# Kernel tuning notes

Hardware: AMD Instinct MI355X
Metric: run time of the kernel (lower is better)

The kernel has to match this reference:

```python
import jax, jax.numpy as jnp
import numpy as np

# Config: B=4, S=2048, E=512, H=8 heads, D=E//H=64, FF=2048.
# QLayer (quantum circuit) is replaced by its linear stand-in matching the
# declared I/O dims: V: D->D per head, Q/K: D->1 (scalar per token).

EPS = 1e-5

def layernorm(x):
    # torch LayerNorm(elementwise_affine=False), population variance
    mu = jnp.mean(x, axis=-1, keepdims=True)
    var = jnp.var(x, axis=-1, keepdims=True)
    return (x - mu) / jnp.sqrt(var + EPS)


def setup_inputs() -> dict:
    key = jax.random.key(0)
    ks = jax.random.split(key, 12)
    B, S, E, H = 4, 2048, 512, 8
    D = E // H
    F = 2048
    u = lambda k, shape, fan: jax.random.uniform(k, shape, jnp.float32, -1.0 / np.sqrt(fan), 1.0 / np.sqrt(fan))
    return {
        "input1": jax.random.normal(ks[0], (B, S, E), jnp.float32),
        # per-head value projection D->D
        "Wv": u(ks[1], (H, D, D), D),
        "bv": u(ks[2], (H, D), D),
        # per-head scalar query / key projections D->1
        "Wq": u(ks[3], (H, D), D),
        "bq": u(ks[4], (H,), D),
        "Wk": u(ks[5], (H, D), D),
        "bk": u(ks[6], (H,), D),
        # merger MLP: E->F (GELU) -> E
        "W1": u(ks[7], (E, F), E),
        "b1": u(ks[8], (F,), E),
        "W2": u(ks[9], (F, E), F),
        "b2": u(ks[10], (E,), F),
    }


def reference(input1, Wv, bv, Wq, bq, Wk, bk, W1, b1, W2, b2):
    B, S, E = input1.shape
    H, D, _ = Wv.shape
    x = layernorm(input1)
    # chunk along last dim == reshape into heads
    xh = x.reshape(B, S, H, D)
    # per-head projections (vectorized over heads)
    V = jnp.einsum('bshd,hde->bshe', xh, Wv) + bv            # [B,S,H,D]
    Q = jnp.einsum('bshd,hd->bhs', xh, Wq) + bq[None, :, None]  # [B,H,S]
    K = jnp.einsum('bshd,hd->bhs', xh, Wk) + bk[None, :, None]  # [B,H,S]
    # quadratic-distance scores: A = -(Q - K)^2, [B,H,S,S]
    A = -jnp.square(Q[:, :, :, None] - K[:, :, None, :])
    attn = jax.nn.softmax(A * (1.0 / np.sqrt(D)), axis=-1)
    head_out = jnp.einsum('bhqk,bkhd->bqhd', attn, V).reshape(B, S, E)
    # merger: Linear -> GELU (exact) -> Linear, plus residual
    h = jax.nn.gelu(head_out @ W1 + b1, approximate=False)
    return h @ W2 + b2 + input1
```

## Files before the change

### kernel.cpp

```cpp
#include <hip/hip_runtime.h>
#include <hip/hip_bf16.h>


#define Bsz 4
#define Ssz 2048
#define Esz 512
#define Hsz 8
#define Dsz 64
#define Fsz 2048
#define NR 16
#define NCH 16
#define CHK 128

typedef __attribute__((ext_vector_type(8))) short bf16x8;
typedef __attribute__((ext_vector_type(4))) float f32x4;

__device__ __constant__ float RS[16] = {
    0.f, 1.0f, 0.70710678f, 0.57735027f, 0.5f, 0.44721360f, 0.40824829f,
    0.37796447f, 0.35355339f, 0.33333333f, 0.31622777f, 0.30151134f,
    0.28867513f, 0.27735010f, 0.26726124f, 0.25819889f};

static __device__ __forceinline__ void gload_lds16(const void* g, void* l) {
    __builtin_amdgcn_global_load_lds(
        (const __attribute__((address_space(1))) unsigned int*)g,
        (__attribute__((address_space(3))) unsigned int*)l, 16, 0, 0);
}

static __device__ __forceinline__ unsigned short f2bf(float f) {
    unsigned int b = __float_as_uint(f);
    b += 0x7FFFu + ((b >> 16) & 1u);
    return (unsigned short)(b >> 16);
}

__global__ __launch_bounds__(256) void ln_qk_kernel(
    const float* __restrict__ x,
    const float* __restrict__ Wq, const float* __restrict__ bq,
    const float* __restrict__ Wk, const float* __restrict__ bk,
    float* __restrict__ Qo, float* __restrict__ Ko, __hip_bfloat16* __restrict__ Xn)
{
    int wid = threadIdx.x >> 6, lane = threadIdx.x & 63;
    int tok = blockIdx.x * 4 + wid;
    int b = tok >> 11, s = tok & 2047;

    const float* xrow = x + (size_t)tok * Esz;
    float4 v0 = *(const float4*)&xrow[lane * 8];
    float4 v1 = *(const float4*)&xrow[lane * 8 + 4];

    float sum = v0.x + v0.y + v0.z + v0.w + v1.x + v1.y + v1.z + v1.w;
    #pragma unroll
    for (int off = 32; off > 0; off >>= 1) sum += __shfl_xor(sum, off);
    float mean = sum * (1.0f / 512.0f);

    float d[8] = {v0.x - mean, v0.y - mean, v0.z - mean, v0.w - mean,
                  v1.x - mean, v1.y - mean, v1.z - mean, v1.w - mean};
    float ss = 0.f;
    #pragma unroll
    for (int j = 0; j < 8; ++j) ss = fmaf(d[j], d[j], ss);
    #pragma unroll
    for (int off = 32; off > 0; off >>= 1) ss += __shfl_xor(ss, off);
    float inv = rsqrtf(ss * (1.0f / 512.0f) + 1e-5f);

    float xn[8];
    #pragma unroll
    for (int j = 0; j < 8; ++j) xn[j] = d[j] * inv;

    int h = lane >> 3, dsub = (lane & 7) * 8;
    union { bf16x8 v; unsigned short u[8]; } pk;
    #pragma unroll
    for (int j = 0; j < 8; ++j) pk.u[j] = f2bf(xn[j]);
    *(bf16x8*)((unsigned short*)Xn + (((size_t)(b * Hsz + h) * Ssz + s) * Dsz + dsub)) = pk.v;

    float4 wqa = *(const float4*)&Wq[h * 64 + dsub];
    float4 wqb = *(const float4*)&Wq[h * 64 + dsub + 4];
    float4 wka = *(const float4*)&Wk[h * 64 + dsub];
    float4 wkb = *(const float4*)&Wk[h * 64 + dsub + 4];
    float pq = xn[0]*wqa.x + xn[1]*wqa.y + xn[2]*wqa.z + xn[3]*wqa.w
             + xn[4]*wqb.x + xn[5]*wqb.y + xn[6]*wqb.z + xn[7]*wqb.w;
    float pkv = xn[0]*wka.x + xn[1]*wka.y + xn[2]*wka.z + xn[3]*wka.w
              + xn[4]*wkb.x + xn[5]*wkb.y + xn[6]*wkb.z + xn[7]*wkb.w;
    #pragma unroll
    for (int off = 1; off < 8; off <<= 1) {
        pq  += __shfl_xor(pq, off);
        pkv += __shfl_xor(pkv, off);
    }
    if ((lane & 7) == 0) {
        int bh = b * Hsz + h;
        Qo[bh * Ssz + s] = pq + bq[h];
        Ko[bh * Ssz + s] = pkv + bk[h];
    }
}

__global__ __launch_bounds__(256) void attn_moments(
    const float* __restrict__ Kv, const __hip_bfloat16* __restrict__ Xn, float* __restrict__ Gp)
{
    int chunk = blockIdx.x, bh = blockIdx.y;
    int t = threadIdx.x;
    __shared__ float Wt[CHK][17];
    __shared__ float denp[4][16];

    if (t < CHK) {
        float kv = Kv[bh * Ssz + chunk * CHK + t];
        float wn = __expf(-0.125f * kv * kv);
        float half = 0.5f * kv;
        Wt[t][0] = wn;
        #pragma unroll
        for (int n = 1; n < NR; ++n) { wn *= half * RS[n]; Wt[t][n] = wn; }
    }
    __syncthreads();

    int w = t >> 6, lane = t & 63;
    int ng = w * 4;
    float a0 = 0.f, a1 = 0.f, a2 = 0.f, a3 = 0.f;
    const __hip_bfloat16* xb = Xn + ((size_t)bh * Ssz + chunk * CHK) * Dsz + lane;
    for (int k = 0; k < CHK; ++k) {
        float v = __bfloat162float(xb[(size_t)k * Dsz]);
        a0 = fmaf(Wt[k][ng + 0], v, a0);
        a1 = fmaf(Wt[k][ng + 1], v, a1);
        a2 = fmaf(Wt[k][ng + 2], v, a2);
        a3 = fmaf(Wt[k][ng + 3], v, a3);
    }
    size_t base = (((size_t)bh * NCH + chunk) * NR + ng) * 68 + lane;
    Gp[base + 0 * 68] = a0;
    Gp[base + 1 * 68] = a1;
    Gp[base + 2 * 68] = a2;
    Gp[base + 3 * 68] = a3;

    if (t < 64) {
        int n = t & 15, q = t >> 4;
        float s = 0.f;
        #pragma unroll
        for (int kk = 0; kk < CHK / 4; ++kk) s += Wt[q * (CHK / 4) + kk][n];
        denp[q][n] = s;
    }
    __syncthreads();
    if (t < 16) {
        float m = denp[0][t] + denp[1][t] + denp[2][t] + denp[3][t];
        Gp[(((size_t)bh * NCH + chunk) * NR + t) * 68 + 64] = m;
    }
}

__global__ __launch_bounds__(256) void attn_mtransform(
    const float* __restrict__ Gp, const float* __restrict__ Wv, const float* __restrict__ bv,
    float* __restrict__ M)
{
    int bh = blockIdx.x, h = bh & 7, t = threadIdx.x;
    __shared__ float Gf[NR * 68];
    for (int i = t; i < NR * 68; i += 256) {
        float s = 0.f;
        #pragma unroll
        for (int c = 0; c < NCH; ++c)
            s += Gp[(((size_t)bh * NCH + c) * NR) * 68 + i];
        Gf[i] = s;
    }
    __syncthreads();
    #pragma unroll
    for (int rep = 0; rep < 4; ++rep) {
        int o = t + rep * 256;
        int n = o >> 6, dd = o & 63;
        float den = Gf[n * 68 + 64];
        float acc = den * bv[h * 64 + dd];
        const float* wv = Wv + ((size_t)h * 64) * 64 + dd;
        #pragma unroll
        for (int e = 0; e < 64; ++e) acc = fmaf(Gf[n * 68 + e], wv[(size_t)e * 64], acc);
        M[(size_t)bh * NR * 68 + n * 68 + dd] = acc;
        if (dd == 0) M[(size_t)bh * NR * 68 + n * 68 + 64] = den;
    }
}

__global__ __launch_bounds__(256) void attn_apply(
    const float* __restrict__ Qv, const float* __restrict__ M, __hip_bfloat16* __restrict__ A1)
{
    int tok = blockIdx.x;
    int b = tok >> 11, s = tok & 2047;
    int t = threadIdx.x;
    #pragma unroll
    for (int rep = 0; rep < 2; ++rep) {
        int e = t + rep * 256;
        int h = e >> 6, dd = e & 63;
        int bh = b * 8 + h;
        float q = Qv[bh * Ssz + s];
        const float* Mb = M + (size_t)bh * NR * 68;
        float half = 0.5f * q;
        float phi = 1.0f;
        float num = Mb[dd], den = Mb[64];
        #pragma unroll
        for (int n = 1; n < NR; ++n) {
            phi *= half * RS[n];
            num = fmaf(phi, Mb[n * 68 + dd], num);
            den = fmaf(phi, Mb[n * 68 + 64], den);
        }
        A1[(size_t)tok * Esz + e] = __float2bfloat16(num / den);
    }
}

__global__ __launch_bounds__(256) void transpose_bf16(
    const float* __restrict__ in, __hip_bfloat16* __restrict__ out, int R, int C)
{
    __shared__ float tile[32][33];
    int bx = blockIdx.x, by = blockIdx.y;
    int t = threadIdx.x;
    int tc = t & 31, tr = t >> 5;
    #pragma unroll
    for (int i = 0; i < 4; ++i) {
        int r = by * 32 + tr + i * 8, c = bx * 32 + tc;
        tile[tr + i * 8][tc] = in[(size_t)r * C + c];
    }
    __syncthreads();
    #pragma unroll
    for (int i = 0; i < 4; ++i) {
        int ro = bx * 32 + tr + i * 8, co = by * 32 + tc;
        out[(size_t)ro * R + co] = __float2bfloat16(tile[tc][tr + i * 8]);
    }
}

template <int KDIM, int EPI>
__global__ __launch_bounds__(256) void gemm_bf16(
    const __hip_bfloat16* __restrict__ A, const __hip_bfloat16* __restrict__ Bt,
    const float* __restrict__ bias, const float* __restrict__ resid,
    void* __restrict__ Out, int N)
{
    __shared__ unsigned short As[128][32];
    __shared__ unsigned short Bs[128][32];
    int t = threadIdx.x;
    int w = t >> 6, lane = t & 63;
    int wr = w >> 1, wc = w & 1;
    int bm = blockIdx.y * 128, bn = blockIdx.x * 128;

    f32x4 acc[4][4] = {};
    const int r = t >> 2, cg = (t & 3) * 8;

    for (int k0 = 0; k0 < KDIM; k0 += 32) {
        gload_lds16(&A[(size_t)(bm + r) * KDIM + k0 + cg], &As[r][cg]);
        gload_lds16(&A[(size_t)(bm + r + 64) * KDIM + k0 + cg], &As[r + 64][cg]);
        gload_lds16(&Bt[(size_t)(bn + r) * KDIM + k0 + cg], &Bs[r][cg]);
        gload_lds16(&Bt[(size_t)(bn + r + 64) * KDIM + k0 + cg], &Bs[r + 64][cg]);
        __syncthreads();
        bf16x8 af[4], bfr[4];
        #pragma unroll
        for (int i = 0; i < 4; ++i) {
            af[i]  = *(const bf16x8*)&As[wr * 64 + i * 16 + (lane & 15)][(lane >> 4) * 8];
            bfr[i] = *(const bf16x8*)&Bs[wc * 64 + i * 16 + (lane & 15)][(lane >> 4) * 8];
        }
        #pragma unroll
        for (int i = 0; i < 4; ++i)
            #pragma unroll
            for (int j = 0; j < 4; ++j)
                acc[i][j] = __builtin_amdgcn_mfma_f32_16x16x32_bf16(af[i], bfr[j], acc[i][j], 0, 0, 0);
        __syncthreads();
    }

    int col0 = lane & 15, rowg = lane >> 4;
    #pragma unroll
    for (int i = 0; i < 4; ++i) {
        #pragma unroll
        for (int j = 0; j < 4; ++j) {
            #pragma unroll
            for (int v = 0; v < 4; ++v) {
                int m = bm + wr * 64 + i * 16 + rowg * 4 + v;
                int n = bn + wc * 64 + j * 16 + col0;
                float val = acc[i][j][v] + bias[n];
                if (EPI == 0) {
                    float g = 0.5f * val * (1.0f + erff(val * 0.70710678f));
                    ((__hip_bfloat16*)Out)[(size_t)m * N + n] = __float2bfloat16(g);
                } else {
                    size_t idx = (size_t)m * N + n;
                    ((float*)Out)[idx] = val + resid[idx];
                }
            }
        }
    }
}

extern "C" void kernel_launch(void* const* d_in, const int* in_sizes, int n_in,
                              void* d_out, int out_size, void* d_ws, size_t ws_size,
                              hipStream_t stream) {
    const float* x  = (const float*)d_in[0];
    const float* Wv = (const float*)d_in[1];
    const float* bv = (const float*)d_in[2];
    const float* Wq = (const float*)d_in[3];
    const float* bq = (const float*)d_in[4];
    const float* Wk = (const float*)d_in[5];
    const float* bk = (const float*)d_in[6];
    const float* W1 = (const float*)d_in[7];
    const float* b1 = (const float*)d_in[8];
    const float* W2 = (const float*)d_in[9];
    const float* b2 = (const float*)d_in[10];
    float* out = (float*)d_out;

    char* ws = (char*)d_ws;
    float* Qb    = (float*)(ws + 0);
    float* Kb    = (float*)(ws + 262144);
    __hip_bfloat16* Xn = (__hip_bfloat16*)(ws + 524288);
    float* Gp    = (float*)(ws + 8912896);
    float* Mfull = (float*)(ws + 11141120);
    __hip_bfloat16* A1   = (__hip_bfloat16*)(ws + 11280384);
    __hip_bfloat16* W1T  = (__hip_bfloat16*)(ws + 19668992);
    __hip_bfloat16* W2T  = (__hip_bfloat16*)(ws + 21766144);
    __hip_bfloat16* hbuf = (__hip_bfloat16*)(ws + 23863296);

    ln_qk_kernel<<<dim3((Bsz * Ssz) / 4), 256, 0, stream>>>(x, Wq, bq, Wk, bk, Qb, Kb, Xn);
    attn_moments<<<dim3(NCH, Bsz * Hsz), 256, 0, stream>>>(Kb, Xn, Gp);
    attn_mtransform<<<dim3(Bsz * Hsz), 256, 0, stream>>>(Gp, Wv, bv, Mfull);
    attn_apply<<<dim3(Bsz * Ssz), 256, 0, stream>>>(Qb, Mfull, A1);
    transpose_bf16<<<dim3(Fsz / 32, Esz / 32), 256, 0, stream>>>(W1, W1T, Esz, Fsz);
    transpose_bf16<<<dim3(Esz / 32, Fsz / 32), 256, 0, stream>>>(W2, W2T, Fsz, Esz);
    gemm_bf16<Esz, 0><<<dim3(Fsz / 128, (Bsz * Ssz) / 128), 256, 0, stream>>>(A1, W1T, b1, nullptr, hbuf, Fsz);
    gemm_bf16<Fsz, 1><<<dim3(Esz / 128, (Bsz * Ssz) / 128), 256, 0, stream>>>(hbuf, W2T, b2, x, out, Esz);
}
```

Before: 210.1 us.

## Fuse prep kernels, merge moments with transform, pipeline GEMMs with triple buffering

Folds layernorm/QK projection and both weight transposes into one prep kernel. Merges the moment computation with the Wv transform using a last-block atomic counter, and vectorizes the moment inner loop with bf16x8 loads and shuffle reductions. Rewrites the GEMM with a 3-stage LDS pipeline using explicit vmcnt waits, a swizzled block order for L2 locality, and a 64-wide N tile for the second GEMM to raise block count. This cuts launches and hides global-load latency, at the cost of more LDS per block and a hand-tuned wait sequence that depends on the exact number of loads in flight.

```diff
diff --git a/kernel.cpp b/kernel.cpp
--- a/kernel.cpp
+++ b/kernel.cpp
@@ -31,75 +31,115 @@
     b += 0x7FFFu + ((b >> 16) & 1u);
     return (unsigned short)(b >> 16);
 }
-
-__global__ __launch_bounds__(256) void ln_qk_kernel(
+static __device__ __forceinline__ float bf2f(unsigned short u) {
+    return __int_as_float(((int)u) << 16);
+}
+
+__global__ __launch_bounds__(256) void prep_kernel(
     const float* __restrict__ x,
     const float* __restrict__ Wq, const float* __restrict__ bq,
     const float* __restrict__ Wk, const float* __restrict__ bk,
-    float* __restrict__ Qo, float* __restrict__ Ko, __hip_bfloat16* __restrict__ Xn)
+    const float* __restrict__ W1, const float* __restrict__ W2,
+    float* __restrict__ Qo, float* __restrict__ Ko, __hip_bfloat16* __restrict__ Xn,
+    __hip_bfloat16* __restrict__ W1T, __hip_bfloat16* __restrict__ W2T)
 {
-    int wid = threadIdx.x >> 6, lane = threadIdx.x & 63;
-    int tok = blockIdx.x * 4 + wid;
-    int b = tok >> 11, s = tok & 2047;
-
-    const float* xrow = x + (size_t)tok * Esz;
-    float4 v0 = *(const float4*)&xrow[lane * 8];
-    float4 v1 = *(const float4*)&xrow[lane * 8 + 4];
-
-    float sum = v0.x + v0.y + v0.z + v0.w + v1.x + v1.y + v1.z + v1.w;
-    #pragma unroll
-    for (int off = 32; off > 0; off >>= 1) sum += __shfl_xor(sum, off);
-    float mean = sum * (1.0f / 512.0f);
-
-    float d[8] = {v0.x - mean, v0.y - mean, v0.z - mean, v0.w - mean,
-                  v1.x - mean, v1.y - mean, v1.z - mean, v1.w - mean};
-    float ss = 0.f;
-    #pragma unroll
-    for (int j = 0; j < 8; ++j) ss = fmaf(d[j], d[j], ss);
-    #pragma unroll
-    for (int off = 32; off > 0; off >>= 1) ss += __shfl_xor(ss, off);
-    float inv = rsqrtf(ss * (1.0f / 512.0f) + 1e-5f);
-
-    float xn[8];
-    #pragma unroll
-    for (int j = 0; j < 8; ++j) xn[j] = d[j] * inv;
-
-    int h = lane >> 3, dsub = (lane & 7) * 8;
-    union { bf16x8 v; unsigned short u[8]; } pk;
-    #pragma unroll
-    for (int j = 0; j < 8; ++j) pk.u[j] = f2bf(xn[j]);
-    *(bf16x8*)((unsigned short*)Xn + (((size_t)(b * Hsz + h) * Ssz + s) * Dsz + dsub)) = pk.v;
-
-    float4 wqa = *(const float4*)&Wq[h * 64 + dsub];
-    float4 wqb = *(const float4*)&Wq[h * 64 + dsub + 4];
-    float4 wka = *(const float4*)&Wk[h * 64 + dsub];
-    float4 wkb = *(const float4*)&Wk[h * 64 + dsub + 4];
-    float pq = xn[0]*wqa.x + xn[1]*wqa.y + xn[2]*wqa.z + xn[3]*wqa.w
-             + xn[4]*wqb.x + xn[5]*wqb.y + xn[6]*wqb.z + xn[7]*wqb.w;
-    float pkv = xn[0]*wka.x + xn[1]*wka.y + xn[2]*wka.z + xn[3]*wka.w
-              + xn[4]*wkb.x + xn[5]*wkb.y + xn[6]*wkb.z + xn[7]*wkb.w;
-    #pragma unroll
-    for (int off = 1; off < 8; off <<= 1) {
-        pq  += __shfl_xor(pq, off);
-        pkv += __shfl_xor(pkv, off);
-    }
-    if ((lane & 7) == 0) {
-        int bh = b * Hsz + h;
-        Qo[bh * Ssz + s] = pq + bq[h];
-        Ko[bh * Ssz + s] = pkv + bk[h];
-    }
-}
-
-__global__ __launch_bounds__(256) void attn_moments(
-    const float* __restrict__ Kv, const __hip_bfloat16* __restrict__ Xn, float* __restrict__ Gp)
+    int bid = blockIdx.x;
+    if (bid < 2048) {
+        int wid = threadIdx.x >> 6, lane = threadIdx.x & 63;
+        int tok = bid * 4 + wid;
+        int b = tok >> 11, s = tok & 2047;
+
+        const float* xrow = x + (size_t)tok * Esz;
+        float4 v0 = *(const float4*)&xrow[lane * 8];
+        float4 v1 = *(const float4*)&xrow[lane * 8 + 4];
+
+        float sum = v0.x + v0.y + v0.z + v0.w + v1.x + v1.y + v1.z + v1.w;
+        #pragma unroll
+        for (int off = 32; off > 0; off >>= 1) sum += __shfl_xor(sum, off);
+        float mean = sum * (1.0f / 512.0f);
+
+        float d[8] = {v0.x - mean, v0.y - mean, v0.z - mean, v0.w - mean,
+                      v1.x - mean, v1.y - mean, v1.z - mean, v1.w - mean};
+        float ss = 0.f;
+        #pragma unroll
+        for (int j = 0; j < 8; ++j) ss = fmaf(d[j], d[j], ss);
+        #pragma unroll
+        for (int off = 32; off > 0; off >>= 1) ss += __shfl_xor(ss, off);
+        float inv = rsqrtf(ss * (1.0f / 512.0f) + 1e-5f);
+
+        float xn[8];
+        #pragma unroll
+        for (int j = 0; j < 8; ++j) xn[j] = d[j] * inv;
+
+        int h = lane >> 3, dsub = (lane & 7) * 8;
+        union { bf16x8 v; unsigned short u[8]; } pk;
+        #pragma unroll
+        for (int j = 0; j < 8; ++j) pk.u[j] = f2bf(xn[j]);
+        *(bf16x8*)((unsigned short*)Xn + (((size_t)(b * Hsz + h) * Ssz + s) * Dsz + dsub)) = pk.v;
+
+        float4 wqa = *(const float4*)&Wq[h * 64 + dsub];
+        float4 wqb = *(const float4*)&Wq[h * 64 + dsub + 4];
+        float4 wka = *(const float4*)&Wk[h * 64 + dsub];
+        float4 wkb = *(const float4*)&Wk[h * 64 + dsub + 4];
+        float pq = xn[0]*wqa.x + xn[1]*wqa.y + xn[2]*wqa.z + xn[3]*wqa.w
+                 + xn[4]*wqb.x + xn[5]*wqb.y + xn[6]*wqb.z + xn[7]*wqb.w;
+        float pkv = xn[0]*wka.x + xn[1]*wka.y + xn[2]*wka.z + xn[3]*wka.w
+                  + xn[4]*wkb.x + xn[5]*wkb.y + xn[6]*wkb.z + xn[7]*wkb.w;
+        #pragma unroll
+        for (int off = 1; off < 8; off <<= 1) {
+            pq  += __shfl_xor(pq, off);
+            pkv += __shfl_xor(pkv, off);
+        }
+        if ((lane & 7) == 0) {
+            int bh = b * Hsz + h;
+            Qo[bh * Ssz + s] = pq + bq[h];
+            Ko[bh * Ssz + s] = pkv + bk[h];
+        }
+        return;
+    }
+
+    __shared__ float tile[32][33];
+    const float* in;
+    __hip_bfloat16* outp;
+    int R, C, bx, by;
+    if (bid < 3072) {
+        int tb = bid - 2048;
+        in = W1; outp = W1T; R = Esz; C = Fsz;
+        bx = tb & 63; by = tb >> 6;
+    } else {
+        int tb = bid - 3072;
+        in = W2; outp = W2T; R = Fsz; C = Esz;
+        bx = tb & 15; by = tb >> 4;
+    }
+    int t = threadIdx.x;
+    int tc = t & 31, tr = t >> 5;
+    #pragma unroll
+    for (int i = 0; i < 4; ++i) {
+        int rr = by * 32 + tr + i * 8, cc = bx * 32 + tc;
+        tile[tr + i * 8][tc] = in[(size_t)rr * C + cc];
+    }
+    __syncthreads();
+    #pragma unroll
+    for (int i = 0; i < 4; ++i) {
+        int ro = bx * 32 + tr + i * 8, co = by * 32 + tc;
+        outp[(size_t)ro * R + co] = __float2bfloat16(tile[tc][tr + i * 8]);
+    }
+}
+
+__global__ __launch_bounds__(256) void attn_moments_fused(
+    const float* __restrict__ Kv, const __hip_bfloat16* __restrict__ Xn,
+    const float* __restrict__ Wv, const float* __restrict__ bvp,
+    float* __restrict__ Gp, float* __restrict__ M, unsigned int* __restrict__ cnt)
 {
-    int chunk = blockIdx.x, bh = blockIdx.y;
+    int bh = blockIdx.x >> 4, chunk = blockIdx.x & 15, h = bh & 7;
     int t = threadIdx.x;
     __shared__ float Wt[CHK][17];
-    __shared__ float denp[4][16];
-
+    __shared__ float Gf[NR * 68];
+    __shared__ int isLast;
+
+    int k0 = chunk * CHK;
     if (t < CHK) {
-        float kv = Kv[bh * Ssz + chunk * CHK + t];
+        float kv = Kv[bh * Ssz + k0 + t];
         float wn = __expf(-0.125f * kv * kv);
         float half = 0.5f * kv;
         Wt[t][0] = wn;
@@ -109,42 +149,56 @@
     __syncthreads();
 
     int w = t >> 6, lane = t & 63;
+    int kk = lane >> 3, dg = lane & 7;
     int ng = w * 4;
-    float a0 = 0.f, a1 = 0.f, a2 = 0.f, a3 = 0.f;
-    const __hip_bfloat16* xb = Xn + ((size_t)bh * Ssz + chunk * CHK) * Dsz + lane;
-    for (int k = 0; k < CHK; ++k) {
-        float v = __bfloat162float(xb[(size_t)k * Dsz]);
-        a0 = fmaf(Wt[k][ng + 0], v, a0);
-        a1 = fmaf(Wt[k][ng + 1], v, a1);
-        a2 = fmaf(Wt[k][ng + 2], v, a2);
-        a3 = fmaf(Wt[k][ng + 3], v, a3);
-    }
-    size_t base = (((size_t)bh * NCH + chunk) * NR + ng) * 68 + lane;
-    Gp[base + 0 * 68] = a0;
-    Gp[base + 1 * 68] = a1;
-    Gp[base + 2 * 68] = a2;
-    Gp[base + 3 * 68] = a3;
-
-    if (t < 64) {
-        int n = t & 15, q = t >> 4;
+    float acc[4][8] = {};
+    const unsigned short* xb = (const unsigned short*)Xn + ((size_t)bh * Ssz + k0) * Dsz + dg * 8;
+    for (int kc = 0; kc < CHK / 8; ++kc) {
+        int kl = kc * 8 + kk;
+        bf16x8 xv = *(const bf16x8*)&xb[(size_t)kl * Dsz];
+        float xf[8];
+        #pragma unroll
+        for (int e = 0; e < 8; ++e) xf[e] = bf2f((unsigned short)xv[e]);
+        #pragma unroll
+        for (int n = 0; n < 4; ++n) {
+            float wt = Wt[kl][ng + n];
+            #pragma unroll
+            for (int e = 0; e < 8; ++e) acc[n][e] = fmaf(wt, xf[e], acc[n][e]);
+        }
+    }
+    #pragma unroll
+    for (int off = 8; off < 64; off <<= 1)
+        #pragma unroll
+        for (int n = 0; n < 4; ++n)
+            #pragma unroll
+            for (int e = 0; e < 8; ++e)
+                acc[n][e] += __shfl_xor(acc[n][e], off);
+    if (kk == 0) {
+        #pragma unroll
+        for (int n = 0; n < 4; ++n) {
+            float* gp = &Gp[(((size_t)bh * NCH + chunk) * NR + ng + n) * 68 + dg * 8];
+            float4 lo = {acc[n][0], acc[n][1], acc[n][2], acc[n][3]};
+            float4 hi = {acc[n][4], acc[n][5], acc[n][6], acc[n][7]};
+            *(float4*)gp = lo;
+            *(float4*)(gp + 4) = hi;
+        }
+    }
+    if (t < NR) {
         float s = 0.f;
-        #pragma unroll
-        for (int kk = 0; kk < CHK / 4; ++kk) s += Wt[q * (CHK / 4) + kk][n];
-        denp[q][n] = s;
-    }
-    __syncthreads();
-    if (t < 16) {
-        float m = denp[0][t] + denp[1][t] + denp[2][t] + denp[3][t];
-        Gp[(((size_t)bh * NCH + chunk) * NR + t) * 68 + 64] = m;
-    }
-}
-
-__global__ __launch_bounds__(256) void attn_mtransform(
-    const float* __restrict__ Gp, const float* __restrict__ Wv, const float* __restrict__ bv,
-    float* __restrict__ M)
-{
-    int bh = blockIdx.x, h = bh & 7, t = threadIdx.x;
-    __shared__ float Gf[NR * 68];
+        for (int k = 0; k < CHK; ++k) s += Wt[k][t];
+        Gp[(((size_t)bh * NCH + chunk) * NR + t) * 68 + 64] = s;
+    }
+
+    __threadfence();
+    __syncthreads();
+    if (t == 0) {
+        unsigned int old = atomicAdd(&cnt[bh], 1u);
+        isLast = (old == NCH - 1) ? 1 : 0;
+    }
+    __syncthreads();
+    if (!isLast) return;
+    __threadfence();
+
     for (int i = t; i < NR * 68; i += 256) {
         float s = 0.f;
         #pragma unroll
@@ -158,11 +212,11 @@
         int o = t + rep * 256;
         int n = o >> 6, dd = o & 63;
         float den = Gf[n * 68 + 64];
-        float acc = den * bv[h * 64 + dd];
+        float accv = den * bvp[h * 64 + dd];
         const float* wv = Wv + ((size_t)h * 64) * 64 + dd;
         #pragma unroll
-        for (int e = 0; e < 64; ++e) acc = fmaf(Gf[n * 68 + e], wv[(size_t)e * 64], acc);
-        M[(size_t)bh * NR * 68 + n * 68 + dd] = acc;
+        for (int e = 0; e < 64; ++e) accv = fmaf(Gf[n * 68 + e], wv[(size_t)e * 64], accv);
+        M[(size_t)bh * NR * 68 + n * 68 + dd] = accv;
         if (dd == 0) M[(size_t)bh * NR * 68 + n * 68 + 64] = den;
     }
 }
@@ -193,77 +247,94 @@
     }
 }
 
-__global__ __launch_bounds__(256) void transpose_bf16(
-    const float* __restrict__ in, __hip_bfloat16* __restrict__ out, int R, int C)
-{
-    __shared__ float tile[32][33];
-    int bx = blockIdx.x, by = blockIdx.y;
-    int t = threadIdx.x;
-    int tc = t & 31, tr = t >> 5;
-    #pragma unroll
-    for (int i = 0; i < 4; ++i) {
-        int r = by * 32 + tr + i * 8, c = bx * 32 + tc;
-        tile[tr + i * 8][tc] = in[(size_t)r * C + c];
-    }
-    __syncthreads();
-    #pragma unroll
-    for (int i = 0; i < 4; ++i) {
-        int ro = bx * 32 + tr + i * 8, co = by * 32 + tc;
-        out[(size_t)ro * R + co] = __float2bfloat16(tile[tc][tr + i * 8]);
-    }
-}
-
-template <int KDIM, int EPI>
+template <int KDIM, int NDIM, int BN, int EPI>
 __global__ __launch_bounds__(256) void gemm_bf16(
     const __hip_bfloat16* __restrict__ A, const __hip_bfloat16* __restrict__ Bt,
     const float* __restrict__ bias, const float* __restrict__ resid,
-    void* __restrict__ Out, int N)
+    void* __restrict__ Out)
 {
-    __shared__ unsigned short As[128][32];
-    __shared__ unsigned short Bs[128][32];
+    constexpr int NT = KDIM / 32;
+    constexpr int NWGX = NDIM / BN;
+    constexpr int NWG = NWGX * 64;
+    constexpr int FN = BN / 32;
+
+    __shared__ unsigned short As[3][128][32];
+    __shared__ unsigned short Bs[3][BN][32];
+
     int t = threadIdx.x;
     int w = t >> 6, lane = t & 63;
     int wr = w >> 1, wc = w & 1;
-    int bm = blockIdx.y * 128, bn = blockIdx.x * 128;
-
-    f32x4 acc[4][4] = {};
+
+    int orig = blockIdx.x;
+    int swz = (orig & 7) * (NWG / 8) + (orig >> 3);
+    int bm = (swz / NWGX) * 128;
+    int bn = (swz % NWGX) * BN;
+
+    f32x4 acc[4][FN] = {};
     const int r = t >> 2, cg = (t & 3) * 8;
 
-    for (int k0 = 0; k0 < KDIM; k0 += 32) {
-        gload_lds16(&A[(size_t)(bm + r) * KDIM + k0 + cg], &As[r][cg]);
-        gload_lds16(&A[(size_t)(bm + r + 64) * KDIM + k0 + cg], &As[r + 64][cg]);
-        gload_lds16(&Bt[(size_t)(bn + r) * KDIM + k0 + cg], &Bs[r][cg]);
-        gload_lds16(&Bt[(size_t)(bn + r + 64) * KDIM + k0 + cg], &Bs[r + 64][cg]);
-        __syncthreads();
-        bf16x8 af[4], bfr[4];
-        #pragma unroll
-        for (int i = 0; i < 4; ++i) {
-            af[i]  = *(const bf16x8*)&As[wr * 64 + i * 16 + (lane & 15)][(lane >> 4) * 8];
-            bfr[i] = *(const bf16x8*)&Bs[wc * 64 + i * 16 + (lane & 15)][(lane >> 4) * 8];
-        }
+    auto stage = [&](int kt, int buf) {
+        int k0 = kt * 32;
+        gload_lds16(&A[(size_t)(bm + r) * KDIM + k0 + cg], &As[buf][r][cg]);
+        gload_lds16(&A[(size_t)(bm + r + 64) * KDIM + k0 + cg], &As[buf][r + 64][cg]);
+        gload_lds16(&Bt[(size_t)(bn + r) * KDIM + k0 + cg], &Bs[buf][r][cg]);
+        if constexpr (BN == 128)
+            gload_lds16(&Bt[(size_t)(bn + r + 64) * KDIM + k0 + cg], &Bs[buf][r + 64][cg]);
+    };
+    auto wait_stage = [&](bool more_inflight) {
+        if (more_inflight) {
+            if constexpr (BN == 128) asm volatile("s_waitcnt vmcnt(4)" ::: "memory");
+            else                     asm volatile("s_waitcnt vmcnt(3)" ::: "memory");
+        } else {
+            asm volatile("s_waitcnt vmcnt(0)" ::: "memory");
+        }
+    };
+
+    stage(0, 0);
+    stage(1, 1);
+    wait_stage(true);
+    __builtin_amdgcn_s_barrier();
+    __builtin_amdgcn_sched_barrier(0);
+
+    for (int kt = 0; kt < NT; ++kt) {
+        int cb = kt % 3;
+        if (kt + 2 < NT) stage(kt + 2, (kt + 2) % 3);
+
+        bf16x8 af[4], bfr[FN];
+        #pragma unroll
+        for (int i = 0; i < 4; ++i)
+            af[i] = *(const bf16x8*)&As[cb][wr * 64 + i * 16 + (lane & 15)][(lane >> 4) * 8];
+        #pragma unroll
+        for (int j = 0; j < FN; ++j)
+            bfr[j] = *(const bf16x8*)&Bs[cb][wc * (BN / 2) + j * 16 + (lane & 15)][(lane >> 4) * 8];
         #pragma unroll
         for (int i = 0; i < 4; ++i)
             #pragma unroll
-            for (int j = 0; j < 4; ++j)
+            for (int j = 0; j < FN; ++j)
                 acc[i][j] = __builtin_amdgcn_mfma_f32_16x16x32_bf16(af[i], bfr[j], acc[i][j], 0, 0, 0);
-        __syncthreads();
+
+        if (kt + 1 < NT) {
+            wait_stage(kt + 2 < NT);
+            __builtin_amdgcn_s_barrier();
+            __builtin_amdgcn_sched_barrier(0);
+        }
     }
 
     int col0 = lane & 15, rowg = lane >> 4;
     #pragma unroll
     for (int i = 0; i < 4; ++i) {
         #pragma unroll
-        for (int j = 0; j < 4; ++j) {
+        for (int j = 0; j < FN; ++j) {
             #pragma unroll
             for (int v = 0; v < 4; ++v) {
                 int m = bm + wr * 64 + i * 16 + rowg * 4 + v;
-                int n = bn + wc * 64 + j * 16 + col0;
+                int n = bn + wc * (BN / 2) + j * 16 + col0;
                 float val = acc[i][j][v] + bias[n];
                 if (EPI == 0) {
                     float g = 0.5f * val * (1.0f + erff(val * 0.70710678f));
-                    ((__hip_bfloat16*)Out)[(size_t)m * N + n] = __float2bfloat16(g);
+                    ((__hip_bfloat16*)Out)[(size_t)m * NDIM + n] = __float2bfloat16(g);
                 } else {
-                    size_t idx = (size_t)m * N + n;
+                    size_t idx = (size_t)m * NDIM + n;
                     ((float*)Out)[idx] = val + resid[idx];
                 }
             }
@@ -292,18 +363,17 @@
     float* Kb    = (float*)(ws + 262144);
     __hip_bfloat16* Xn = (__hip_bfloat16*)(ws + 524288);
     float* Gp    = (float*)(ws + 8912896);
-    float* Mfull = (float*)(ws + 11141120);
-    __hip_bfloat16* A1   = (__hip_bfloat16*)(ws + 11280384);
-    __hip_bfloat16* W1T  = (__hip_bfloat16*)(ws + 19668992);
-    __hip_bfloat16* W2T  = (__hip_bfloat16*)(ws + 21766144);
-    __hip_bfloat16* hbuf = (__hip_bfloat16*)(ws + 23863296);
-
-    ln_qk_kernel<<<dim3((Bsz * Ssz) / 4), 256, 0, stream>>>(x, Wq, bq, Wk, bk, Qb, Kb, Xn);
-    attn_moments<<<dim3(NCH, Bsz * Hsz), 256, 0, stream>>>(Kb, Xn, Gp);
-    attn_mtransform<<<dim3(Bsz * Hsz), 256, 0, stream>>>(Gp, Wv, bv, Mfull);
+    __hip_bfloat16* A1 = (__hip_bfloat16*)(ws + 8912896);
+    float* Mfull = (float*)(ws + 17301504);
+    unsigned int* cnt = (unsigned int*)(ws + 17440768);
+    __hip_bfloat16* W1T  = (__hip_bfloat16*)(ws + 17441024);
+    __hip_bfloat16* W2T  = (__hip_bfloat16*)(ws + 19538176);
+    __hip_bfloat16* hbuf = (__hip_bfloat16*)(ws + 21635328);
+
+    hipMemsetAsync(cnt, 0, 32 * sizeof(unsigned int), stream);
+    prep_kernel<<<dim3(4096), 256, 0, stream>>>(x, Wq, bq, Wk, bk, W1, W2, Qb, Kb, Xn, W1T, W2T);
+    attn_moments_fused<<<dim3(Bsz * Hsz * NCH), 256, 0, stream>>>(Kb, Xn, Wv, bv, Gp, Mfull, cnt);
     attn_apply<<<dim3(Bsz * Ssz), 256, 0, stream>>>(Qb, Mfull, A1);
-    transpose_bf16<<<dim3(Fsz / 32, Esz / 32), 256, 0, stream>>>(W1, W1T, Esz, Fsz);
-    transpose_bf16<<<dim3(Esz / 32, Fsz / 32), 256, 0, stream>>>(W2, W2T, Fsz, Esz);
-    gemm_bf16<Esz, 0><<<dim3(Fsz / 128, (Bsz * Ssz) / 128), 256, 0, stream>>>(A1, W1T, b1, nullptr, hbuf, Fsz);
-    gemm_bf16<Fsz, 1><<<dim3(Esz / 128, (Bsz * Ssz) / 128), 256, 0, stream>>>(hbuf, W2T, b2, x, out, Esz);
-}
+    gemm_bf16<Esz, Fsz, 128, 0><<<dim3(1024), 256, 0, stream>>>(A1, W1T, b1, nullptr, hbuf);
+    gemm_bf16<Fsz, Esz, 64, 1><<<dim3(512), 256, 0, stream>>>(hbuf, W2T, b2, x, out);
+}
```

After: 267.7 us. 1.27x slower.
